# Performance work log

Measured on AMD Instinct MI355X. Metric: run time of the kernel, lower is better.

The kernel has to match this reference:

```python
import jax, jax.numpy as jnp
import numpy as np

N_NODES, N_EDGES = 16000, 256000
M_IN_S, M_IN_V = 16, 8   # input irreps: 16x0e + 8x1o (dim 40)
M_K_S, M_K_V = 8, 4      # key/query irreps: 8x0e + 4x1o
M_V_S, M_V_V = 16, 8     # value irreps: 16x0e + 8x1o
NUM_BASIS, R_CUT = 32, 2.5
SQ3 = 1.7320508075688772  # sqrt(3)


def _fc_net(r, W1, W2):
    # e3nn FullyConnectedNet([num_basis,16,numels], silu): weight-normalized linears
    h = jax.nn.silu(r @ (W1 / jnp.sqrt(jnp.float32(W1.shape[0]))))
    return h @ (W2 / jnp.sqrt(jnp.float32(W2.shape[0])))


def _edge_tp(xs, xv, y0, y1, w, m1s, m1v, mos, mov):
    # FullyConnectedTensorProduct(in1 = m1s x0e + m1v x1o, in2 = 1x0e + 1x1o,
    #   out = mos x0e + mov x1o), per-edge external weights w [E, numels].
    # Paths: 0e*0e->0e, 1o*1o->0e (dot/sqrt3), 0e*1o->1o, 1o*0e->1o.
    E = w.shape[0]
    n1, n2, n3 = m1s * mos, m1v * mos, m1s * mov
    w_ss = w[:, :n1].reshape(E, m1s, mos)
    w_vv = w[:, n1:n1 + n2].reshape(E, m1v, mos)
    w_sv = w[:, n1 + n2:n1 + n2 + n3].reshape(E, m1s, mov)
    w_vs = w[:, n1 + n2 + n3:].reshape(E, m1v, mov)
    inv = 1.0 / jnp.sqrt(jnp.float32(m1s + m1v))  # fan-in path normalization
    out_s = (jnp.einsum('ei,eio->eo', xs * y0[:, None], w_ss)
             + jnp.einsum('eic,ec,eio->eo', xv, y1, w_vv) / SQ3) * inv
    out_v = (jnp.einsum('ei,ec,eio->eoc', xs, y1, w_sv)
             + jnp.einsum('eic,eio->eoc', xv * y0[:, None, None], w_vs)) * inv
    return out_s, out_v


def _forward(pos, x, Wq_s, Wq_v, Wk1, Wk2, Wv1, Wv2, Ws_ss, Ws_vv, edge_src, edge_dst):
    xs, xv = x[:, :M_IN_S], x[:, M_IN_S:].reshape(-1, M_IN_V, 3)
    vec = pos[edge_dst] - pos[edge_src]                       # [E,3]
    d = jnp.linalg.norm(vec, axis=1)
    d_safe = jnp.maximum(d, 1e-6)
    # bessel radial basis with cutoff (soft_one_hot_linspace, basis='bessel') * sqrt(num_basis)
    n = jnp.arange(1, NUM_BASIS + 1, dtype=jnp.float32)
    rad = jnp.sqrt(2.0 / R_CUT) * jnp.sin(n[None] * jnp.pi * d_safe[:, None] / R_CUT) / d_safe[:, None]
    rad = jnp.where((d < R_CUT)[:, None], rad, 0.0) * jnp.sqrt(jnp.float32(NUM_BASIS))
    # spherical harmonics lmax=1, normalize=True, component normalization
    vh = vec / d_safe[:, None]
    y0, y1 = jnp.ones_like(d), SQ3 * vh
    # query projection (o3.Linear: per-irrep linear with 1/sqrt(fan_in))
    q_s = xs @ Wq_s / jnp.sqrt(jnp.float32(M_IN_S))           # [N, M_K_S]
    q_v = jnp.einsum('nic,io->noc', xv, Wq_v) / jnp.sqrt(jnp.float32(M_IN_V))
    # per-edge tensor-product weights from radial MLPs (shared_weights=False)
    wk = _fc_net(rad, Wk1, Wk2)                               # [E, 288]
    wv = _fc_net(rad, Wv1, Wv2)                               # [E, 576]
    xs_e, xv_e = xs[edge_src], xv[edge_src]
    k_s, k_v = _edge_tp(xs_e, xv_e, y0, y1, wk, M_IN_S, M_IN_V, M_K_S, M_K_V)
    v_s, v_v = _edge_tp(xs_e, xv_e, y0, y1, wv, M_IN_S, M_IN_V, M_V_S, M_V_V)
    # similarity tensor product (query x key -> 0e), shared internal weights
    fan = jnp.sqrt(jnp.float32(M_K_S * M_K_S + M_K_V * M_K_V))
    sim = (jnp.einsum('ei,ij,ej->e', q_s[edge_dst], Ws_ss, k_s)
           + jnp.einsum('eic,ij,ejc->e', q_v[edge_dst], Ws_vv, k_v) / SQ3) / fan
    # scatter softmax over incoming edges of each dst node
    attn = jnp.exp(sim)
    Z = jax.ops.segment_sum(attn, edge_dst, num_segments=N_NODES)
    a = attn / Z[edge_dst]
    # weighted scatter-sum aggregation
    out_s = jax.ops.segment_sum(a[:, None] * v_s, edge_dst, num_segments=N_NODES)
    out_v = jax.ops.segment_sum(a[:, None, None] * v_v, edge_dst, num_segments=N_NODES)
    return jnp.concatenate([out_s, out_v.reshape(N_NODES, -1)], axis=1)  # [N, 40]


def setup_inputs() -> dict:
    key = jax.random.key(0)
    ks = jax.random.split(key, 12)
    wk_numels = M_IN_S * M_K_S + M_IN_V * M_K_S + M_IN_S * M_K_V + M_IN_V * M_K_V  # 288
    wv_numels = M_IN_S * M_V_S + M_IN_V * M_V_S + M_IN_S * M_V_V + M_IN_V * M_V_V  # 576
    return {
        'pos': jax.random.uniform(ks[0], (N_NODES, 3), jnp.float32) * 3.0,
        'x': jax.random.normal(ks[1], (N_NODES, M_IN_S + 3 * M_IN_V), jnp.float32),
        'Wq_s': jax.random.normal(ks[2], (M_IN_S, M_K_S), jnp.float32),
        'Wq_v': jax.random.normal(ks[3], (M_IN_V, M_K_V), jnp.float32),
        'Wk1': jax.random.normal(ks[4], (NUM_BASIS, 16), jnp.float32),
        'Wk2': jax.random.normal(ks[5], (16, wk_numels), jnp.float32),
        'Wv1': jax.random.normal(ks[6], (NUM_BASIS, 16), jnp.float32),
        'Wv2': jax.random.normal(ks[7], (16, wv_numels), jnp.float32),
        'Ws_ss': jax.random.normal(ks[8], (M_K_S, M_K_S), jnp.float32) * 0.1,
        'Ws_vv': jax.random.normal(ks[9], (M_K_V, M_K_V), jnp.float32) * 0.1,
        'edge_src': jax.random.randint(ks[10], (N_EDGES,), 0, N_NODES),
        'edge_dst': jax.random.randint(ks[11], (N_EDGES,), 0, N_NODES),
    }


def reference(pos, x, Wq_s, Wq_v, Wk1, Wk2, Wv1, Wv2, Ws_ss, Ws_vv, edge_src, edge_dst):
    return _forward(pos, x, Wq_s, Wq_v, Wk1, Wk2, Wv1, Wv2, Ws_ss, Ws_vv, edge_src, edge_dst)
```

## Files before the change

### kernel.cpp

```cpp
#include <hip/hip_runtime.h>
#include <hip/hip_bf16.h>

#define N_NODES 16000
#define N_EDGES 256000

#define OFF_SD     0
#define OFF_SIMB   512000
#define OFF_CNT    768000
#define OFF_START  784000
#define OFF_CUR    800001
#define OFF_WB     816004
#define OFF_WBK    834436
#define OFF_QT     846724
#define OFF_Z      1006724

typedef _Float16 f16x2 __attribute__((ext_vector_type(2)));
typedef _Float16 f16x8v __attribute__((ext_vector_type(8)));
typedef float f32x4v __attribute__((ext_vector_type(4)));

__device__ __forceinline__ float fdot2f(f16x2 a, f16x2 b, float c) {
#if __has_builtin(__builtin_amdgcn_fdot2)
  return __builtin_amdgcn_fdot2(a, b, c, false);
#else
  return fmaf((float)a.x, (float)b.x, fmaf((float)a.y, (float)b.y, c));
#endif
}

__device__ __forceinline__ unsigned packh2(float a, float b) {
  union { unsigned u; f16x2 p; } v;
  v.p.x = (_Float16)a; v.p.y = (_Float16)b;
  return v.u;
}

__device__ __forceinline__ unsigned splat_half(unsigned x, unsigned sel) {
#if __has_builtin(__builtin_amdgcn_perm)
  return __builtin_amdgcn_perm(x, x, sel);
#else
  unsigned h = (sel == 0x03020302u) ? (x >> 16) : (x & 0xffffu);
  return h | (h << 16);
#endif
}

__device__ __forceinline__ void load_row40(const float* __restrict__ p, float* xr) {
  const float4* rp = reinterpret_cast<const float4*>(p);
#pragma unroll
  for (int q = 0; q < 10; ++q) {
    float4 f = rp[q];
    xr[4 * q + 0] = f.x; xr[4 * q + 1] = f.y; xr[4 * q + 2] = f.z; xr[4 * q + 3] = f.w;
  }
}

struct EdgeGeom { float vhx, vhy, vhz, y1x, y1y, y1z; };

__device__ __forceinline__ void edge_h_pk(const float* __restrict__ pos, int s, int d,
                                          const unsigned* W1, f16x2* hp, EdgeGeom& g) {
  float vx = pos[3 * d + 0] - pos[3 * s + 0];
  float vy = pos[3 * d + 1] - pos[3 * s + 1];
  float vz = pos[3 * d + 2] - pos[3 * s + 2];
  float dist = sqrtf(fmaf(vx, vx, fmaf(vy, vy, vz * vz)));
  float dsafe = fmaxf(dist, 1e-6f);
  float rinv = 1.0f / dsafe;
  g.vhx = vx * rinv; g.vhy = vy * rinv; g.vhz = vz * rinv;
  g.y1x = 1.7320508075688772f * g.vhx;
  g.y1y = 1.7320508075688772f * g.vhy;
  g.y1z = 1.7320508075688772f * g.vhz;
  float pre[16];
#pragma unroll
  for (int t = 0; t < 16; ++t) pre[t] = 0.f;
  float sx, cx;
  sincosf(1.2566370614359172f * dsafe, &sx, &cx);
  cx = fminf(1.f, fmaxf(-1.f, cx));
  float twoc = 2.f * cx;
  float sprev = 0.f, scur = sx;
  float rscale = (dist < 2.5f) ? (5.059644256269407f * rinv) : 0.f;
#pragma unroll
  for (int bp = 0; bp < 16; ++bp) {
    float r0 = rscale * scur;
    float sn = fmaf(twoc, scur, -sprev); sprev = scur; scur = sn;
    float r1 = rscale * scur;
    sn = fmaf(twoc, scur, -sprev); sprev = scur; scur = sn;
    union { unsigned u; f16x2 p; } rp; rp.p.x = (_Float16)r0; rp.p.y = (_Float16)r1;
    union { uint4 u[4]; f16x2 p[16]; } w;
    w.u[0] = *(const uint4*)(W1 + bp * 16);
    w.u[1] = *(const uint4*)(W1 + bp * 16 + 4);
    w.u[2] = *(const uint4*)(W1 + bp * 16 + 8);
    w.u[3] = *(const uint4*)(W1 + bp * 16 + 12);
#pragma unroll
    for (int t = 0; t < 16; ++t) pre[t] = fdot2f(rp.p, w.p[t], pre[t]);
  }
#pragma unroll
  for (int tp = 0; tp < 8; ++tp) {
    float h0 = pre[2 * tp]     / (1.f + __expf(-pre[2 * tp]));
    float h1 = pre[2 * tp + 1] / (1.f + __expf(-pre[2 * tp + 1]));
    hp[tp].x = (_Float16)h0; hp[tp].y = (_Float16)h1;
  }
}

__global__ void k_hist(const int* __restrict__ edst, int* __restrict__ cnt) {
  int e = blockIdx.x * 256 + threadIdx.x;
  atomicAdd(&cnt[edst[e]], 1);
}

__global__ void __launch_bounds__(1024) k_scan(const int* __restrict__ cnt,
                                               int* __restrict__ start, int* __restrict__ cur) {
  __shared__ int part[1024];
  int t = threadIdx.x;
  int base = t * 16;
  int local[16];
  int sum = 0;
#pragma unroll
  for (int i = 0; i < 16; ++i) {
    int idx = base + i;
    int c = (idx < N_NODES) ? cnt[idx] : 0;
    local[i] = sum; sum += c;
  }
  part[t] = sum;
  __syncthreads();
  for (int off = 1; off < 1024; off <<= 1) {
    int v = (t >= off) ? part[t - off] : 0;
    __syncthreads();
    part[t] += v;
    __syncthreads();
  }
  int prev = (t == 0) ? 0 : part[t - 1];
#pragma unroll
  for (int i = 0; i < 16; ++i) {
    int idx = base + i;
    if (idx < N_NODES) { int st = prev + local[i]; start[idx] = st; cur[idx] = st; }
  }
  if (t == 0) start[N_NODES] = N_EDGES;
}

__global__ void k_fill(const int* __restrict__ esrc, const int* __restrict__ edst,
                       int* __restrict__ cur, int2* __restrict__ sd) {
  int e = blockIdx.x * 256 + threadIdx.x;
  int d = edst[e];
  int slot = atomicAdd(&cur[d], 1);
  sd[slot] = make_int2(esrc[e], d);
}

__global__ void k_prepB(const float* __restrict__ Wv2, unsigned short* __restrict__ WB) {
  int idx = blockIdx.x * 256 + threadIdx.x;
  int j = idx & 7;
  int lane = (idx >> 3) & 63;
  int t3 = idx >> 9;
  int ct = t3 % 3, kk = t3 / 3;
  int q = lane >> 4, m = lane & 15;
  int row = 32 * kk + 8 * q + j;
  int col = 16 * ct + m;
  int t = row & 15;
  float v = 0.f;
  if (row < 256) {
    int i = row >> 4;
    if (col < 16)      v = Wv2[t * 576 + i * 16 + col];
    else if (col < 24) v = Wv2[t * 576 + 384 + i * 8 + (col - 16)];
  } else if (row < 384) {
    int i = (row - 256) >> 4;
    if (col < 16)      v = Wv2[t * 576 + 256 + i * 16 + col];
  } else {
    int part = (row - 384) >> 7;
    int i = ((row - 384) & 127) >> 4;
    int cb = 24 + 8 * part;
    if (col >= cb && col < cb + 8) v = Wv2[t * 576 + 512 + i * 8 + (col - cb)];
  }
  union { unsigned short u; _Float16 h; } cv;
  cv.h = (_Float16)(v * 0.051031036307982884f);
  WB[idx] = cv.u;
}

__global__ void k_prepBK(const float* __restrict__ Wk2, unsigned short* __restrict__ WBK) {
  int idx = blockIdx.x * 256 + threadIdx.x;
  int j = idx & 7;
  int lane = (idx >> 3) & 63;
  int t2 = idx >> 9;
  int ct = t2 & 1, kk = t2 >> 1;
  int q = lane >> 4, m = lane & 15;
  int row = 32 * kk + 8 * q + j;
  int col = 16 * ct + m;
  int t = row & 15;
  float v = 0.f;
  if (col < 24) {
    if (row < 256) {
      int i = row >> 4;
      if (col < 8)       v = Wk2[t * 288 + i * 8 + col];
      else if (col < 12) v = Wk2[t * 288 + 192 + i * 4 + (col - 8)];
    } else if (row < 384) {
      int i = (row - 256) >> 4;
      if (col < 8)       v = Wk2[t * 288 + 128 + i * 8 + col];
    } else {
      int c = (row - 384) >> 7;
      int i = ((row - 384) & 127) >> 4;
      int cb = 12 + 4 * c;
      if (col >= cb && col < cb + 4) v = Wk2[t * 288 + 256 + i * 4 + (col - cb)];
    }
  }
  union { unsigned short u; _Float16 h; } cv;
  cv.h = (_Float16)(v * 0.051031036307982884f);
  WBK[idx] = cv.u;
}

__global__ void __launch_bounds__(128) k_nodeq(
    const float* __restrict__ x,
    const float* __restrict__ Wq_s, const float* __restrict__ Wq_v,
    const float* __restrict__ Wss, const float* __restrict__ Wvv,
    unsigned short* __restrict__ QT) {
  __shared__ float Ls[240];
  for (int i = threadIdx.x; i < 240; i += 128) {
    float v;
    if (i < 128)      v = Wq_s[i] * 0.25f;
    else if (i < 160) v = Wq_v[i - 128] * 0.3535533905932738f;
    else if (i < 224) v = Wss[i - 160] * 0.11180339887498948f;
    else              v = Wvv[i - 224] * 0.06454972243679028f;
    Ls[i] = v;
  }
  __syncthreads();
  int n = blockIdx.x * 128 + threadIdx.x;
  float xd[40];
  load_row40(x + 40 * n, xd);
  float qd[8], qvd[12];
#pragma unroll
  for (int o = 0; o < 8; ++o) qd[o] = 0.f;
#pragma unroll
  for (int i = 0; i < 16; ++i)
#pragma unroll
    for (int o = 0; o < 8; ++o) qd[o] = fmaf(xd[i], Ls[8 * i + o], qd[o]);
#pragma unroll
  for (int k = 0; k < 12; ++k) qvd[k] = 0.f;
#pragma unroll
  for (int i = 0; i < 8; ++i)
#pragma unroll
    for (int o = 0; o < 4; ++o)
#pragma unroll
      for (int c = 0; c < 3; ++c)
        qvd[3 * o + c] = fmaf(xd[16 + 3 * i + c], Ls[128 + 4 * i + o], qvd[3 * o + c]);
  float qf[20];
#pragma unroll
  for (int j = 0; j < 8; ++j) {
    float t = 0.f;
#pragma unroll
    for (int i = 0; i < 8; ++i) t = fmaf(qd[i], Ls[160 + 8 * i + j], t);
    qf[j] = t;
  }
#pragma unroll
  for (int o = 0; o < 4; ++o)
#pragma unroll
    for (int c = 0; c < 3; ++c) {
      float t = 0.f;
#pragma unroll
      for (int i = 0; i < 4; ++i) t = fmaf(qvd[3 * i + c], Ls[224 + 4 * i + o], t);
      qf[8 + 3 * o + c] = t;
    }
  uint2* qp = (uint2*)(QT + 20 * n);
#pragma unroll
  for (int b = 0; b < 5; ++b) {
    uint2 st;
    st.x = packh2(qf[4 * b], qf[4 * b + 1]);
    st.y = packh2(qf[4 * b + 2], qf[4 * b + 3]);
    qp[b] = st;
  }
}

#define RSTR 36

__device__ __forceinline__ void build_coef(const float* xr, const float* Bv, float* coef) {
#pragma unroll
  for (int i = 0; i < 16; ++i) coef[i] = xr[i];
#pragma unroll
  for (int i = 0; i < 8; ++i) coef[16 + i] = Bv[i];
#pragma unroll
  for (int p = 0; p < 4; ++p)
#pragma unroll
    for (int c = 0; c < 3; ++c) {
      coef[24 + 8 * c + 2 * p]     = xr[16 + 6 * p + c];
      coef[24 + 8 * c + 2 * p + 1] = xr[16 + 6 * p + 3 + c];
    }
}

__global__ void __launch_bounds__(256) k_edge1(
    const float* __restrict__ pos, const float* __restrict__ x,
    const float* __restrict__ Wk1, const unsigned short* __restrict__ WBK,
    const unsigned short* __restrict__ QT,
    const int2* __restrict__ sd, float* __restrict__ simb, float* __restrict__ Z) {
  __shared__ __align__(16) unsigned LW1[256];
  __shared__ __align__(16) unsigned SM[4][64 * RSTR];

  for (int i = threadIdx.x; i < 256; i += 256) {
    int bp = i >> 4, t = i & 15;
    LW1[i] = packh2(Wk1[(2 * bp) * 16 + t] * 0.17677669529663687f,
                    Wk1[(2 * bp + 1) * 16 + t] * 0.17677669529663687f);
  }
  __syncthreads();

  int wave = threadIdx.x >> 6, lane = threadIdx.x & 63;
  int q = lane >> 4, m = lane & 15;
  int q1 = q & 1;
  unsigned seld = (q >> 1) ? 0x03020302u : 0x01000100u;
  int slot = blockIdx.x * 256 + threadIdx.x;
  int2 e = sd[slot];
  int s = e.x, d = e.y;

  f16x2 hp[8]; EdgeGeom g;
  edge_h_pk(pos, s, d, LW1, hp, g);

  float qf[20];
  {
    const uint2* qp = (const uint2*)(QT + 20 * d);
#pragma unroll
    for (int b = 0; b < 5; ++b) {
      uint2 u = qp[b];
      union { unsigned d; f16x2 p; } a0, a1;
      a0.d = u.x; a1.d = u.y;
      qf[4 * b] = (float)a0.p.x; qf[4 * b + 1] = (float)a0.p.y;
      qf[4 * b + 2] = (float)a1.p.x; qf[4 * b + 3] = (float)a1.p.y;
    }
  }

  float xr[40];
  load_row40(x + 40 * s, xr);
  float Bv[8];
#pragma unroll
  for (int i = 0; i < 8; ++i)
    Bv[i] = fmaf(xr[16 + 3 * i], g.vhx, fmaf(xr[17 + 3 * i], g.vhy, xr[18 + 3 * i] * g.vhz));
  float coef[48];
  build_coef(xr, Bv, coef);

  unsigned* row = &SM[wave][lane * RSTR];
  {
    union { uint4 u; f16x2 p[4]; } h0, h1;
#pragma unroll
    for (int k = 0; k < 4; ++k) { h0.p[k] = hp[k]; h1.p[k] = hp[4 + k]; }
    *(uint4*)(row) = h0.u;
    *(uint4*)(row + 4) = h1.u;
  }
#pragma unroll
  for (int bt = 0; bt < 6; ++bt) {
    uint4 w;
    w.x = packh2(coef[8 * bt + 0], coef[8 * bt + 1]);
    w.y = packh2(coef[8 * bt + 2], coef[8 * bt + 3]);
    w.z = packh2(coef[8 * bt + 4], coef[8 * bt + 5]);
    w.w = packh2(coef[8 * bt + 6], coef[8 * bt + 7]);
    *(uint4*)(row + 8 + 4 * bt) = w;
  }
  unsigned* wbase = &SM[wave][0];
  union { uint4 u; f16x2 p[4]; } hs[4];
#pragma unroll
  for (int rt = 0; rt < 4; ++rt)
    hs[rt].u = *(const uint4*)(wbase + (16 * rt + m) * RSTR + 4 * q1);

  const uint4* WBq = (const uint4*)WBK;
  f32x4v acc[4][2];
#pragma unroll
  for (int rt = 0; rt < 4; ++rt)
#pragma unroll
    for (int ct = 0; ct < 2; ++ct) { f32x4v z = {0.f, 0.f, 0.f, 0.f}; acc[rt][ct] = z; }

#pragma unroll
  for (int bt = 0; bt < 6; ++bt) {
    union { uint4 u; unsigned d[4]; } cb[4];
#pragma unroll
    for (int rt = 0; rt < 4; ++rt)
      cb[rt].u = *(const uint4*)(wbase + (16 * rt + m) * RSTR + 8 + 4 * bt);
#pragma unroll
    for (int t = 0; t < 4; ++t) {
      int kk = 4 * bt + t;
      union { uint4 u; f16x2 p[4]; f16x8v v; } av[4];
#pragma unroll
      for (int rt = 0; rt < 4; ++rt) {
        union { unsigned d; f16x2 p; } sp;
        sp.d = splat_half(cb[rt].d[t], seld);
#pragma unroll
        for (int w = 0; w < 4; ++w) av[rt].p[w] = hs[rt].p[w] * sp.p;
      }
#pragma unroll
      for (int ct = 0; ct < 2; ++ct) {
        union { uint4 u; f16x8v v; } bf;
        bf.u = WBq[(kk * 2 + ct) * 64 + lane];
#pragma unroll
        for (int rt = 0; rt < 4; ++rt)
          acc[rt][ct] = __builtin_amdgcn_mfma_f32_16x16x32_f16(av[rt].v, bf.v, acc[rt][ct], 0, 0, 0);
      }
    }
  }

  float P[24];
  float* ctb = (float*)wbase;
#pragma unroll
  for (int rt = 0; rt < 4; ++rt)
#pragma unroll
    for (int r = 0; r < 4; ++r)
      ctb[m * 65 + 16 * rt + 4 * q + r] = acc[rt][0][r];
#pragma unroll
  for (int o = 0; o < 16; ++o) P[o] = ctb[o * 65 + lane];
#pragma unroll
  for (int rt = 0; rt < 4; ++rt)
#pragma unroll
    for (int r = 0; r < 4; ++r)
      ctb[m * 65 + 16 * rt + 4 * q + r] = acc[rt][1][r];
#pragma unroll
  for (int o = 0; o < 8; ++o) P[16 + o] = ctb[o * 65 + lane];

  float sim = 0.f;
#pragma unroll
  for (int j = 0; j < 8; ++j) sim = fmaf(qf[j], P[j], sim);
  float y1c[3] = {g.y1x, g.y1y, g.y1z};
#pragma unroll
  for (int o = 0; o < 4; ++o)
#pragma unroll
    for (int c = 0; c < 3; ++c)
      sim = fmaf(qf[8 + 3 * o + c], fmaf(y1c[c], P[8 + o], P[12 + 4 * c + o]), sim);

  float ev = __expf(sim);
  simb[slot] = ev;
  bool same[6];
#pragma unroll
  for (int k = 0; k < 6; ++k) {
    int dd = __shfl_down(d, 1 << k, 64);
    same[k] = ((lane + (1 << k)) < 64) && (dd == d);
  }
  int dprev = __shfl_up(d, 1, 64);
  bool head = (lane == 0) || (dprev != d);
  float v = ev;
#pragma unroll
  for (int k = 0; k < 6; ++k) {
    float ov = __shfl_down(v, 1 << k, 64);
    v += same[k] ? ov : 0.f;
  }
  if (head) atomicAdd(&Z[d], v);
}

__global__ void __launch_bounds__(256) k_edge2(
    const float* __restrict__ pos, const float* __restrict__ x,
    const float* __restrict__ Wv1, const unsigned short* __restrict__ WB,
    const int2* __restrict__ sd, const float* __restrict__ eb,
    const float* __restrict__ Zv, float* __restrict__ out) {
  __shared__ __align__(16) unsigned LW1[256];
  __shared__ __align__(16) unsigned SM[4][64 * RSTR];

  for (int i = threadIdx.x; i < 256; i += 256) {
    int bp = i >> 4, t = i & 15;
    LW1[i] = packh2(Wv1[(2 * bp) * 16 + t] * 0.17677669529663687f,
                    Wv1[(2 * bp + 1) * 16 + t] * 0.17677669529663687f);
  }
  __syncthreads();

  int wave = threadIdx.x >> 6, lane = threadIdx.x & 63;
  int q = lane >> 4, m = lane & 15;
  int q1 = q & 1;
  unsigned seld = (q >> 1) ? 0x03020302u : 0x01000100u;
  int slot = blockIdx.x * 256 + threadIdx.x;
  int2 e = sd[slot];
  int s = e.x, d = e.y;

  float ev = eb[slot];
  float Zd = Zv[d];

  bool same[6];
#pragma unroll
  for (int k = 0; k < 6; ++k) {
    int dd = __shfl_down(d, 1 << k, 64);
    same[k] = ((lane + (1 << k)) < 64) && (dd == d);
  }
  int dprev = __shfl_up(d, 1, 64);
  bool head = (lane == 0) || (dprev != d);

  f16x2 hp[8]; EdgeGeom g;
  edge_h_pk(pos, s, d, LW1, hp, g);
  float xr[40];
  load_row40(x + 40 * s, xr);
  float Bv[8];
#pragma unroll
  for (int i = 0; i < 8; ++i)
    Bv[i] = fmaf(xr[16 + 3 * i], g.vhx, fmaf(xr[17 + 3 * i], g.vhy, xr[18 + 3 * i] * g.vhz));
  float coef[48];
  build_coef(xr, Bv, coef);
  float a = ev / Zd;

  unsigned* row = &SM[wave][lane * RSTR];
  {
    union { uint4 u; f16x2 p[4]; } h0, h1;
#pragma unroll
    for (int k = 0; k < 4; ++k) { h0.p[k] = hp[k]; h1.p[k] = hp[4 + k]; }
    *(uint4*)(row) = h0.u;
    *(uint4*)(row + 4) = h1.u;
  }
#pragma unroll
  for (int bt = 0; bt < 6; ++bt) {
    uint4 w;
    w.x = packh2(coef[8 * bt + 0], coef[8 * bt + 1]);
    w.y = packh2(coef[8 * bt + 2], coef[8 * bt + 3]);
    w.z = packh2(coef[8 * bt + 4], coef[8 * bt + 5]);
    w.w = packh2(coef[8 * bt + 6], coef[8 * bt + 7]);
    *(uint4*)(row + 8 + 4 * bt) = w;
  }
  unsigned* wbase = &SM[wave][0];
  union { uint4 u; f16x2 p[4]; } hs[4];
#pragma unroll
  for (int rt = 0; rt < 4; ++rt)
    hs[rt].u = *(const uint4*)(wbase + (16 * rt + m) * RSTR + 4 * q1);

  const uint4* WBq = (const uint4*)WB;
  f32x4v acc[4][3];
#pragma unroll
  for (int rt = 0; rt < 4; ++rt)
#pragma unroll
    for (int ct = 0; ct < 3; ++ct) { f32x4v z = {0.f, 0.f, 0.f, 0.f}; acc[rt][ct] = z; }

#pragma unroll
  for (int bt = 0; bt < 6; ++bt) {
    union { uint4 u; unsigned d[4]; } cb[4];
#pragma unroll
    for (int rt = 0; rt < 4; ++rt)
      cb[rt].u = *(const uint4*)(wbase + (16 * rt + m) * RSTR + 8 + 4 * bt);
#pragma unroll
    for (int t = 0; t < 4; ++t) {
      int kk = 4 * bt + t;
      union { uint4 u; f16x2 p[4]; f16x8v v; } av[4];
#pragma unroll
      for (int rt = 0; rt < 4; ++rt) {
        union { unsigned d; f16x2 p; } sp;
        sp.d = splat_half(cb[rt].d[t], seld);
#pragma unroll
        for (int w = 0; w < 4; ++w) av[rt].p[w] = hs[rt].p[w] * sp.p;
      }
#pragma unroll
      for (int ct = 0; ct < 3; ++ct) {
        union { uint4 u; f16x8v v; } bf;
        bf.u = WBq[(kk * 3 + ct) * 64 + lane];
#pragma unroll
        for (int rt = 0; rt < 4; ++rt)
          acc[rt][ct] = __builtin_amdgcn_mfma_f32_16x16x32_f16(av[rt].v, bf.v, acc[rt][ct], 0, 0, 0);
      }
    }
  }

  float* ctb = (float*)wbase;
  float* op = out + 40 * d;

  {
#pragma unroll
    for (int rt = 0; rt < 4; ++rt)
#pragma unroll
      for (int r = 0; r < 4; ++r)
        ctb[m * 65 + 16 * rt + 4 * q + r] = acc[rt][0][r];
    float P0[16];
#pragma unroll
    for (int o = 0; o < 16; ++o) P0[o] = ctb[o * 65 + lane];
#pragma unroll
    for (int o = 0; o < 16; ++o) {
      float v = a * P0[o];
#pragma unroll
      for (int k = 0; k < 6; ++k) {
        float ov = __shfl_down(v, 1 << k, 64);
        v += same[k] ? ov : 0.f;
      }
      if (head) atomicAdd(op + o, v);
    }
  }
  float P1[16], P2[16];
#pragma unroll
  for (int rt = 0; rt < 4; ++rt)
#pragma unroll
    for (int r = 0; r < 4; ++r)
      ctb[m * 65 + 16 * rt + 4 * q + r] = acc[rt][1][r];
#pragma unroll
  for (int o = 0; o < 16; ++o) P1[o] = ctb[o * 65 + lane];
#pragma unroll
  for (int rt = 0; rt < 4; ++rt)
#pragma unroll
    for (int r = 0; r < 4; ++r)
      ctb[m * 65 + 16 * rt + 4 * q + r] = acc[rt][2][r];
#pragma unroll
  for (int o = 0; o < 16; ++o) P2[o] = ctb[o * 65 + lane];
#pragma unroll
  for (int o = 0; o < 8; ++o) {
    float s1v = P1[o];
    float vc[3];
    vc[0] = a * fmaf(g.y1x, s1v, P1[8 + o]);
    vc[1] = a * fmaf(g.y1y, s1v, P2[o]);
    vc[2] = a * fmaf(g.y1z, s1v, P2[8 + o]);
#pragma unroll
    for (int c = 0; c < 3; ++c) {
      float v = vc[c];
#pragma unroll
      for (int k = 0; k < 6; ++k) {
        float ov = __shfl_down(v, 1 << k, 64);
        v += same[k] ? ov : 0.f;
      }
      if (head) atomicAdd(op + 16 + 3 * o + c, v);
    }
  }
}

extern "C" void kernel_launch(void* const* d_in, const int* in_sizes, int n_in,
                              void* d_out, int out_size, void* d_ws, size_t ws_size,
                              hipStream_t stream) {
  (void)in_sizes; (void)n_in; (void)out_size; (void)ws_size;
  const float* pos  = (const float*)d_in[0];
  const float* x    = (const float*)d_in[1];
  const float* Wq_s = (const float*)d_in[2];
  const float* Wq_v = (const float*)d_in[3];
  const float* Wk1  = (const float*)d_in[4];
  const float* Wk2  = (const float*)d_in[5];
  const float* Wv1  = (const float*)d_in[6];
  const float* Wv2  = (const float*)d_in[7];
  const float* Wss  = (const float*)d_in[8];
  const float* Wvv  = (const float*)d_in[9];
  const int* esrc = (const int*)d_in[10];
  const int* edst = (const int*)d_in[11];
  int*   wsi  = (int*)d_ws;
  float* wsf  = (float*)d_ws;
  float* out  = (float*)d_out;

  int2*  sd    = (int2*)(wsi + OFF_SD);
  float* simb  = wsf + OFF_SIMB;
  int*   cnt   = wsi + OFF_CNT;
  int*   start = wsi + OFF_START;
  int*   cur   = wsi + OFF_CUR;
  unsigned short* WB  = (unsigned short*)(wsf + OFF_WB);
  unsigned short* WBK = (unsigned short*)(wsf + OFF_WBK);
  unsigned short* QT  = (unsigned short*)(wsf + OFF_QT);
  float* Z    = wsf + OFF_Z;

  hipMemsetAsync(cnt, 0, (size_t)N_NODES * sizeof(int), stream);
  hipMemsetAsync(Z, 0, (size_t)N_NODES * sizeof(float), stream);
  hipMemsetAsync(out, 0, (size_t)(N_NODES * 40) * sizeof(float), stream);
  k_prepB<<<144, 256, 0, stream>>>(Wv2, WB);
  k_prepBK<<<96, 256, 0, stream>>>(Wk2, WBK);
  k_nodeq<<<125, 128, 0, stream>>>(x, Wq_s, Wq_v, Wss, Wvv, QT);
  k_hist<<<1000, 256, 0, stream>>>(edst, cnt);
  k_scan<<<1, 1024, 0, stream>>>(cnt, start, cur);
  k_fill<<<1000, 256, 0, stream>>>(esrc, edst, cur, sd);
  k_edge1<<<1000, 256, 0, stream>>>(pos, x, Wk1, WBK, QT, sd, simb, Z);
  k_edge2<<<1000, 256, 0, stream>>>(pos, x, Wv1, WB, sd, simb, Z, out);
}
```

Before: 225.8 us.

## Fuse memsets and prep kernels into one launch; shrink edge blocks to one wave

```diff
diff --git a/kernel.cpp b/kernel.cpp
--- a/kernel.cpp
+++ b/kernel.cpp
@@ -139,73 +139,94 @@
   sd[slot] = make_int2(esrc[e], d);
 }
 
-__global__ void k_prepB(const float* __restrict__ Wv2, unsigned short* __restrict__ WB) {
-  int idx = blockIdx.x * 256 + threadIdx.x;
-  int j = idx & 7;
-  int lane = (idx >> 3) & 63;
-  int t3 = idx >> 9;
-  int ct = t3 % 3, kk = t3 / 3;
-  int q = lane >> 4, m = lane & 15;
-  int row = 32 * kk + 8 * q + j;
-  int col = 16 * ct + m;
-  int t = row & 15;
-  float v = 0.f;
-  if (row < 256) {
-    int i = row >> 4;
-    if (col < 16)      v = Wv2[t * 576 + i * 16 + col];
-    else if (col < 24) v = Wv2[t * 576 + 384 + i * 8 + (col - 16)];
-  } else if (row < 384) {
-    int i = (row - 256) >> 4;
-    if (col < 16)      v = Wv2[t * 576 + 256 + i * 16 + col];
-  } else {
-    int part = (row - 384) >> 7;
-    int i = ((row - 384) & 127) >> 4;
-    int cb = 24 + 8 * part;
-    if (col >= cb && col < cb + 8) v = Wv2[t * 576 + 512 + i * 8 + (col - cb)];
-  }
-  union { unsigned short u; _Float16 h; } cv;
-  cv.h = (_Float16)(v * 0.051031036307982884f);
-  WB[idx] = cv.u;
-}
-
-__global__ void k_prepBK(const float* __restrict__ Wk2, unsigned short* __restrict__ WBK) {
-  int idx = blockIdx.x * 256 + threadIdx.x;
-  int j = idx & 7;
-  int lane = (idx >> 3) & 63;
-  int t2 = idx >> 9;
-  int ct = t2 & 1, kk = t2 >> 1;
-  int q = lane >> 4, m = lane & 15;
-  int row = 32 * kk + 8 * q + j;
-  int col = 16 * ct + m;
-  int t = row & 15;
-  float v = 0.f;
-  if (col < 24) {
-    if (row < 256) {
-      int i = row >> 4;
-      if (col < 8)       v = Wk2[t * 288 + i * 8 + col];
-      else if (col < 12) v = Wk2[t * 288 + 192 + i * 4 + (col - 8)];
-    } else if (row < 384) {
-      int i = (row - 256) >> 4;
-      if (col < 8)       v = Wk2[t * 288 + 128 + i * 8 + col];
-    } else {
-      int c = (row - 384) >> 7;
-      int i = ((row - 384) & 127) >> 4;
-      int cb = 12 + 4 * c;
-      if (col >= cb && col < cb + 4) v = Wk2[t * 288 + 256 + i * 4 + (col - cb)];
-    }
-  }
-  union { unsigned short u; _Float16 h; } cv;
-  cv.h = (_Float16)(v * 0.051031036307982884f);
-  WBK[idx] = cv.u;
-}
-
-__global__ void __launch_bounds__(128) k_nodeq(
+#define PREP_ZERO_B   2625
+#define PREP_PB_B     144
+#define PREP_PBK_B    96
+#define PREP_NQ_B     63
+#define PREP_TOTAL_B  (PREP_ZERO_B + PREP_PB_B + PREP_PBK_B + PREP_NQ_B)
+
+__global__ void __launch_bounds__(256) k_prep(
     const float* __restrict__ x,
     const float* __restrict__ Wq_s, const float* __restrict__ Wq_v,
     const float* __restrict__ Wss, const float* __restrict__ Wvv,
+    const float* __restrict__ Wk2, const float* __restrict__ Wv2,
+    int* __restrict__ cnt, float* __restrict__ Z, float* __restrict__ out,
+    unsigned short* __restrict__ WB, unsigned short* __restrict__ WBK,
     unsigned short* __restrict__ QT) {
+  int b = blockIdx.x;
+  if (b < PREP_ZERO_B) {
+    int i = b * 256 + threadIdx.x;
+    if (i < 16000)       cnt[i] = 0;
+    else if (i < 32000)  Z[i - 16000] = 0.f;
+    else                 out[i - 32000] = 0.f;
+    return;
+  }
+  b -= PREP_ZERO_B;
+  if (b < PREP_PB_B) {
+    int idx = b * 256 + threadIdx.x;
+    int j = idx & 7;
+    int lane = (idx >> 3) & 63;
+    int t3 = idx >> 9;
+    int ct = t3 % 3, kk = t3 / 3;
+    int q = lane >> 4, m = lane & 15;
+    int row = 32 * kk + 8 * q + j;
+    int col = 16 * ct + m;
+    int t = row & 15;
+    float v = 0.f;
+    if (row < 256) {
+      int i = row >> 4;
+      if (col < 16)      v = Wv2[t * 576 + i * 16 + col];
+      else if (col < 24) v = Wv2[t * 576 + 384 + i * 8 + (col - 16)];
+    } else if (row < 384) {
+      int i = (row - 256) >> 4;
+      if (col < 16)      v = Wv2[t * 576 + 256 + i * 16 + col];
+    } else {
+      int part = (row - 384) >> 7;
+      int i = ((row - 384) & 127) >> 4;
+      int cb = 24 + 8 * part;
+      if (col >= cb && col < cb + 8) v = Wv2[t * 576 + 512 + i * 8 + (col - cb)];
+    }
+    union { unsigned short u; _Float16 h; } cv;
+    cv.h = (_Float16)(v * 0.051031036307982884f);
+    WB[idx] = cv.u;
+    return;
+  }
+  b -= PREP_PB_B;
+  if (b < PREP_PBK_B) {
+    int idx = b * 256 + threadIdx.x;
+    int j = idx & 7;
+    int lane = (idx >> 3) & 63;
+    int t2 = idx >> 9;
+    int ct = t2 & 1, kk = t2 >> 1;
+    int q = lane >> 4, m = lane & 15;
+    int row = 32 * kk + 8 * q + j;
+    int col = 16 * ct + m;
+    int t = row & 15;
+    float v = 0.f;
+    if (col < 24) {
+      if (row < 256) {
+        int i = row >> 4;
+        if (col < 8)       v = Wk2[t * 288 + i * 8 + col];
+        else if (col < 12) v = Wk2[t * 288 + 192 + i * 4 + (col - 8)];
+      } else if (row < 384) {
+        int i = (row - 256) >> 4;
+        if (col < 8)       v = Wk2[t * 288 + 128 + i * 8 + col];
+      } else {
+        int c = (row - 384) >> 7;
+        int i = ((row - 384) & 127) >> 4;
+        int cb = 12 + 4 * c;
+        if (col >= cb && col < cb + 4) v = Wk2[t * 288 + 256 + i * 4 + (col - cb)];
+      }
+    }
+    union { unsigned short u; _Float16 h; } cv;
+    cv.h = (_Float16)(v * 0.051031036307982884f);
+    WBK[idx] = cv.u;
+    return;
+  }
+  b -= PREP_PBK_B;
   __shared__ float Ls[240];
-  for (int i = threadIdx.x; i < 240; i += 128) {
+  if (threadIdx.x < 240) {
+    int i = threadIdx.x;
     float v;
     if (i < 128)      v = Wq_s[i] * 0.25f;
     else if (i < 160) v = Wq_v[i - 128] * 0.3535533905932738f;
@@ -214,7 +235,8 @@
     Ls[i] = v;
   }
   __syncthreads();
-  int n = blockIdx.x * 128 + threadIdx.x;
+  int n = b * 256 + threadIdx.x;
+  if (n >= N_NODES) return;
   float xd[40];
   load_row40(x + 40 * n, xd);
   float qd[8], qvd[12];
@@ -252,11 +274,11 @@
     }
   uint2* qp = (uint2*)(QT + 20 * n);
 #pragma unroll
-  for (int b = 0; b < 5; ++b) {
+  for (int bq = 0; bq < 5; ++bq) {
     uint2 st;
-    st.x = packh2(qf[4 * b], qf[4 * b + 1]);
-    st.y = packh2(qf[4 * b + 2], qf[4 * b + 3]);
-    qp[b] = st;
+    st.x = packh2(qf[4 * bq], qf[4 * bq + 1]);
+    st.y = packh2(qf[4 * bq + 2], qf[4 * bq + 3]);
+    qp[bq] = st;
   }
 }
 
@@ -276,26 +298,26 @@
     }
 }
 
-__global__ void __launch_bounds__(256) k_edge1(
+__global__ void __launch_bounds__(64) k_edge1(
     const float* __restrict__ pos, const float* __restrict__ x,
     const float* __restrict__ Wk1, const unsigned short* __restrict__ WBK,
     const unsigned short* __restrict__ QT,
     const int2* __restrict__ sd, float* __restrict__ simb, float* __restrict__ Z) {
   __shared__ __align__(16) unsigned LW1[256];
-  __shared__ __align__(16) unsigned SM[4][64 * RSTR];
-
-  for (int i = threadIdx.x; i < 256; i += 256) {
+  __shared__ __align__(16) unsigned SM[64 * RSTR];
+
+  for (int i = threadIdx.x; i < 256; i += 64) {
     int bp = i >> 4, t = i & 15;
     LW1[i] = packh2(Wk1[(2 * bp) * 16 + t] * 0.17677669529663687f,
                     Wk1[(2 * bp + 1) * 16 + t] * 0.17677669529663687f);
   }
   __syncthreads();
 
-  int wave = threadIdx.x >> 6, lane = threadIdx.x & 63;
+  int lane = threadIdx.x;
   int q = lane >> 4, m = lane & 15;
   int q1 = q & 1;
   unsigned seld = (q >> 1) ? 0x03020302u : 0x01000100u;
-  int slot = blockIdx.x * 256 + threadIdx.x;
+  int slot = blockIdx.x * 64 + threadIdx.x;
   int2 e = sd[slot];
   int s = e.x, d = e.y;
 
@@ -324,7 +346,7 @@
   float coef[48];
   build_coef(xr, Bv, coef);
 
-  unsigned* row = &SM[wave][lane * RSTR];
+  unsigned* row = &SM[lane * RSTR];
   {
     union { uint4 u; f16x2 p[4]; } h0, h1;
 #pragma unroll
@@ -341,7 +363,7 @@
     w.w = packh2(coef[8 * bt + 6], coef[8 * bt + 7]);
     *(uint4*)(row + 8 + 4 * bt) = w;
   }
-  unsigned* wbase = &SM[wave][0];
+  unsigned* wbase = &SM[0];
   union { uint4 u; f16x2 p[4]; } hs[4];
 #pragma unroll
   for (int rt = 0; rt < 4; ++rt)
@@ -428,26 +450,26 @@
   if (head) atomicAdd(&Z[d], v);
 }
 
-__global__ void __launch_bounds__(256) k_edge2(
+__global__ void __launch_bounds__(64) k_edge2(
     const float* __restrict__ pos, const float* __restrict__ x,
     const float* __restrict__ Wv1, const unsigned short* __restrict__ WB,
     const int2* __restrict__ sd, const float* __restrict__ eb,
     const float* __restrict__ Zv, float* __restrict__ out) {
   __shared__ __align__(16) unsigned LW1[256];
-  __shared__ __align__(16) unsigned SM[4][64 * RSTR];
-
-  for (int i = threadIdx.x; i < 256; i += 256) {
+  __shared__ __align__(16) unsigned SM[64 * RSTR];
+
+  for (int i = threadIdx.x; i < 256; i += 64) {
     int bp = i >> 4, t = i & 15;
     LW1[i] = packh2(Wv1[(2 * bp) * 16 + t] * 0.17677669529663687f,
                     Wv1[(2 * bp + 1) * 16 + t] * 0.17677669529663687f);
   }
   __syncthreads();
 
-  int wave = threadIdx.x >> 6, lane = threadIdx.x & 63;
+  int lane = threadIdx.x;
   int q = lane >> 4, m = lane & 15;
   int q1 = q & 1;
   unsigned seld = (q >> 1) ? 0x03020302u : 0x01000100u;
-  int slot = blockIdx.x * 256 + threadIdx.x;
+  int slot = blockIdx.x * 64 + threadIdx.x;
   int2 e = sd[slot];
   int s = e.x, d = e.y;
 
@@ -475,7 +497,7 @@
   build_coef(xr, Bv, coef);
   float a = ev / Zd;
 
-  unsigned* row = &SM[wave][lane * RSTR];
+  unsigned* row = &SM[lane * RSTR];
   {
     union { uint4 u; f16x2 p[4]; } h0, h1;
 #pragma unroll
@@ -492,7 +514,7 @@
     w.w = packh2(coef[8 * bt + 6], coef[8 * bt + 7]);
     *(uint4*)(row + 8 + 4 * bt) = w;
   }
-  unsigned* wbase = &SM[wave][0];
+  unsigned* wbase = &SM[0];
   union { uint4 u; f16x2 p[4]; } hs[4];
 #pragma unroll
   for (int rt = 0; rt < 4; ++rt)
@@ -621,15 +643,11 @@
   unsigned short* QT  = (unsigned short*)(wsf + OFF_QT);
   float* Z    = wsf + OFF_Z;
 
-  hipMemsetAsync(cnt, 0, (size_t)N_NODES * sizeof(int), stream);
-  hipMemsetAsync(Z, 0, (size_t)N_NODES * sizeof(float), stream);
-  hipMemsetAsync(out, 0, (size_t)(N_NODES * 40) * sizeof(float), stream);
-  k_prepB<<<144, 256, 0, stream>>>(Wv2, WB);
-  k_prepBK<<<96, 256, 0, stream>>>(Wk2, WBK);
-  k_nodeq<<<125, 128, 0, stream>>>(x, Wq_s, Wq_v, Wss, Wvv, QT);
+  k_prep<<<PREP_TOTAL_B, 256, 0, stream>>>(x, Wq_s, Wq_v, Wss, Wvv, Wk2, Wv2,
+                                           cnt, Z, out, WB, WBK, QT);
   k_hist<<<1000, 256, 0, stream>>>(edst, cnt);
   k_scan<<<1, 1024, 0, stream>>>(cnt, start, cur);
   k_fill<<<1000, 256, 0, stream>>>(esrc, edst, cur, sd);
-  k_edge1<<<1000, 256, 0, stream>>>(pos, x, Wk1, WBK, QT, sd, simb, Z);
-  k_edge2<<<1000, 256, 0, stream>>>(pos, x, Wv1, WB, sd, simb, Z, out);
-}
+  k_edge1<<<4000, 64, 0, stream>>>(pos, x, Wk1, WBK, QT, sd, simb, Z);
+  k_edge2<<<4000, 64, 0, stream>>>(pos, x, Wv1, WB, sd, simb, Z, out);
+}
```

Measured after the change: 220.2 us. 1.03x faster.
